# Kernel tuning notes

Measured on AMD Instinct MI355X. Metric: run time of the kernel, lower is better.

## Reference

```python
import jax, jax.numpy as jnp
import numpy as np
from jax import lax

B, CIN, COUT, K, MOD, BANK = 4, 64, 32, 3, 128, 4
D = H = W = 32
EPS = 1e-8


def _lin_upsample2x(x, axis):
    n = x.shape[axis]
    dst = jnp.arange(2 * n, dtype=jnp.float32)
    src = jnp.maximum((dst + 0.5) * 0.5 - 0.5, 0.0)
    i0 = jnp.floor(src).astype(jnp.int32)
    i1 = jnp.minimum(i0 + 1, n - 1)
    w1 = src - i0.astype(jnp.float32)
    shape = [1] * x.ndim
    shape[axis] = 2 * n
    w1 = w1.reshape(shape)
    return jnp.take(x, i0, axis=axis) * (1.0 - w1) + jnp.take(x, i1, axis=axis) * w1


def upsample_trilinear2x(x):
    for ax in (2, 3, 4):
        x = _lin_upsample2x(x, ax)
    return x


def setup_inputs() -> dict:
    key = jax.random.key(0)
    ks = jax.random.split(key, 9)
    fan = CIN * K * K * K
    return {
        "x": jax.random.normal(ks[0], (B, CIN, D, H, W), jnp.float32),
        "style": jax.random.normal(ks[1], (B, MOD), jnp.float32),
        "bank": jax.random.normal(ks[2], (BANK, COUT, CIN, K, K, K), jnp.float32) / np.sqrt(fan),
        "affine_w": jax.random.normal(ks[3], (CIN, MOD), jnp.float32) / np.sqrt(MOD),
        "affine_b": jnp.ones((CIN,), jnp.float32),  # StyleGAN bias init = 1
        "sel_w": jax.random.normal(ks[4], (BANK, MOD), jnp.float32) / np.sqrt(MOD),
        "sel_b": jnp.zeros((BANK,), jnp.float32),
        "vox_w": jax.random.normal(ks[5], (1, COUT), jnp.float32) / np.sqrt(COUT),
        "vox_b": jnp.zeros((1,), jnp.float32),
    }


def reference(x, style, bank, affine_w, affine_b, sel_w, sel_b, vox_w, vox_b):
    # --- AdaptiveModulatedConv3d: select kernel from bank, modulate, demodulate ---
    alpha = jax.nn.softmax(style @ sel_w.T + sel_b, axis=-1)            # [B, BANK]
    w = jnp.einsum('bn,noidhw->boidhw', alpha, bank)                    # per-sample kernel
    s = style @ affine_w.T + affine_b                                   # [B, CIN]
    w = w * s[:, None, :, None, None, None]                             # modulate
    demod = lax.rsqrt(jnp.sum(w * w, axis=(2, 3, 4, 5)) + EPS)          # [B, COUT]
    w = w * demod[:, :, None, None, None, None]

    def conv1(xi, wi):
        return lax.conv_general_dilated(
            xi[None], wi, window_strides=(1, 1, 1),
            padding=[(1, 1), (1, 1), (1, 1)],
            dimension_numbers=('NCDHW', 'OIDHW', 'NCDHW'))[0]

    y = jax.vmap(conv1)(x, w)                                           # [B, COUT, D, H, W]

    y = upsample_trilinear2x(y)                                         # [B, COUT, 2D, 2H, 2W]

    # --- VoxelizingBlock: 1x1x1 conv to 1 channel ---
    out = jnp.einsum('oc,bcdhw->bodhw', vox_w, y) + vox_b[None, :, None, None, None]
    return (y, out)
```

## Files before the change

kernel.cpp:

```cpp
#include <hip/hip_runtime.h>
#include <math.h>

#define B_    4
#define CIN_  64
#define COUT_ 32
#define MOD_  128
#define VOX_  32768
#define UPVOX_ 262144
#define TAPS_ 27
#define EPS_  1e-8f

#define HALO_   1224
#define XUNITS_ 2448
#define CHUNK_HALVES_ 13824

#define WS_WF16  512
#define WS_Y     111104
#define WS_V32   4305408

#define OUT_YUP  0
#define OUT_VOX  33554432

typedef _Float16 half8 __attribute__((ext_vector_type(8)));
typedef float floatx16 __attribute__((ext_vector_type(16)));
typedef float floatx4 __attribute__((ext_vector_type(4)));

__global__ __launch_bounds__(256) void k_prep(
    const float* __restrict__ x,
    const float* __restrict__ style,
    const float* __restrict__ bank,
    const float* __restrict__ affine_w,
    const float* __restrict__ affine_b,
    const float* __restrict__ sel_w,
    const float* __restrict__ sel_b,
    _Float16* __restrict__ xt,
    _Float16* __restrict__ wf) {
  __shared__ float red[256];
  __shared__ float sS[64];
  __shared__ float sLg[4];
  __shared__ float sAl[4];
  const int tid = threadIdx.x;

  if (blockIdx.z == 4) {
    const int sid = blockIdx.y * 34 + blockIdx.x;
    if (sid >= 128) return;
    const int b = sid >> 5;
    const int o = sid & 31;
    const float* st = style + b * MOD_;

    if (tid < 64) {
      float v = affine_b[tid];
      for (int k = 0; k < MOD_; ++k) v += st[k] * affine_w[tid * MOD_ + k];
      sS[tid] = v;
    } else if (tid < 68) {
      const int n = tid - 64;
      float l = sel_b[n];
      for (int k = 0; k < MOD_; ++k) l += st[k] * sel_w[n * MOD_ + k];
      sLg[n] = l;
    }
    __syncthreads();
    if (tid < 4) {
      const float m = fmaxf(fmaxf(sLg[0], sLg[1]), fmaxf(sLg[2], sLg[3]));
      float den = 0.f;
      for (int j = 0; j < 4; ++j) den += expf(sLg[j] - m);
      sAl[tid] = expf(sLg[tid] - m) / den;
    }
    __syncthreads();

    float al[4];
#pragma unroll
    for (int n = 0; n < 4; ++n) al[n] = sAl[n];

    float wv[7];
    float ss = 0.f;
#pragma unroll
    for (int r = 0; r < 7; ++r) {
      const int e = tid + r * 256;
      float v = 0.f;
      if (e < CIN_ * TAPS_) {
        const int i = e / TAPS_;
        const int t = e - i * TAPS_;
        const int base = (o * CIN_ + i) * TAPS_ + t;
        float bw = 0.f;
#pragma unroll
        for (int n = 0; n < 4; ++n)
          bw += al[n] * bank[base + n * (COUT_ * CIN_ * TAPS_)];
        v = bw * sS[i];
      }
      wv[r] = v;
      ss += v * v;
    }
    red[tid] = ss;
    __syncthreads();
    for (int stg = 128; stg > 0; stg >>= 1) {
      if (tid < stg) red[tid] += red[tid + stg];
      __syncthreads();
    }
    const float demod = rsqrtf(red[0] + EPS_);

#pragma unroll
    for (int r = 0; r < 7; ++r) {
      const int e = tid + r * 256;
      if (e < CIN_ * TAPS_) {
        const int i = e / TAPS_;
        const int t = e - i * TAPS_;
        const int c = i >> 4, h = (i >> 3) & 1, j = i & 7;
        wf[((((b * 4 + c) * TAPS_ + t) * 2 + h) * 32 + o) * 8 + j] =
            (_Float16)(wv[r] * demod);
      }
    }
    return;
  }

  const int yp = blockIdx.x, zp = blockIdx.y, b = blockIdx.z;
  const int gz = zp - 1, gy = yp - 1;
  const bool zy_ok = ((unsigned)gz < 32u) && ((unsigned)gy < 32u);
  const int gzc = min(max(gz, 0), 31);
  const int gyc = min(max(gy, 0), 31);
  _Float16* dst = xt + (((size_t)(b * 34 + zp) * 34 + yp) * 34) * 64;
  const float* srow = x + ((size_t)b * CIN_) * VOX_ + gzc * 1024 + gyc * 32;
  for (int u = tid; u < 34 * 8; u += 256) {
    const int xp = u >> 3, q = u & 7;
    const int gx = xp - 1;
    const bool ok = zy_ok && ((unsigned)gx < 32u);
    const float m = ok ? 1.0f : 0.0f;
    const int gxc = min(max(gx, 0), 31);
    half8 h;
#pragma unroll
    for (int i = 0; i < 8; ++i) {
      const float v = srow[(size_t)(q * 8 + i) * VOX_ + gxc];
      h[i] = (_Float16)(v * m);
    }
    *(half8*)&dst[xp * 64 + q * 8] = h;
  }
}

__global__ __launch_bounds__(256, 1) void k_conv(
    const _Float16* __restrict__ xt,
    const _Float16* __restrict__ wf,
    const float* __restrict__ vox_w,
    float* __restrict__ ws_y,
    float* __restrict__ v32) {
  __shared__ __align__(16) _Float16 xs[2][XUNITS_ * 8];

  const int b  = blockIdx.y;
  const int bx = blockIdx.x;
  const int z0 = (bx >> 3) * 4;
  const int y0 = (bx & 7) * 4;
  const int tid = threadIdx.x;
  const int w = tid >> 6;
  const int lane = tid & 63;
  const int hf = lane >> 5;
  const int col = lane & 31;
  const int wz = (w >> 1) * 2;
  const int wy = (w & 1) * 2;

  const _Float16* xtb = xt + (size_t)b * (34 * 34 * 34 * 64);
  const _Float16* wfb = wf + (size_t)b * 4 * CHUNK_HALVES_;
  const _Float16* wlane = wfb + ((size_t)(hf * 32 + col)) * 8;

  int xoff[10];
  bool xok[10];
#pragma unroll
  for (int j = 0; j < 10; ++j) {
    const int u = j * 256 + tid;
    xok[j] = (u < XUNITS_);
    const int uc = xok[j] ? u : 0;
    const int h = uc / HALO_, hv = uc - h * HALO_;
    const int hz = hv / 204;
    const int rem = hv - hz * 204;
    const int hy = rem / 34;
    const int hx = rem - hy * 34;
    xoff[j] = (((z0 + hz) * 34 + (y0 + hy)) * 34 + hx) * 64 + h * 8;
  }

  floatx16 acc[2][2];
#pragma unroll
  for (int az = 0; az < 2; ++az)
#pragma unroll
    for (int ay = 0; ay < 2; ++ay)
#pragma unroll
      for (int r = 0; r < 16; ++r) acc[az][ay][r] = 0.f;

  half8 xv[10], afv[27];

  auto load_af = [&](int c) {
#pragma unroll
    for (int t = 0; t < TAPS_; ++t)
      afv[t] = *(const half8*)(wlane + (size_t)c * CHUNK_HALVES_ + t * 512);
  };
  auto load_chunk = [&](int c) {
#pragma unroll
    for (int j = 0; j < 10; ++j)
      xv[j] = *(const half8*)(xtb + xoff[j] + c * 16);
  };
  auto write_chunk = [&](int bufi) {
#pragma unroll
    for (int j = 0; j < 10; ++j) {
      const int u = j * 256 + tid;
      if (xok[j]) *(half8*)&xs[bufi][u * 8] = xv[j];
    }
  };
  auto compute = [&](int bufi) {
    const _Float16* xb_ = xs[bufi];
#pragma unroll
    for (int dx = 0; dx < 3; ++dx) {
      half8 Bf[4][4];
#pragma unroll
      for (int zs = 0; zs < 4; ++zs)
#pragma unroll
        for (int ys = 0; ys < 4; ++ys) {
          const int hv = ((wz + zs) * 6 + (wy + ys)) * 34 + dx + col;
          Bf[zs][ys] = *(const half8*)&xb_[(hf * HALO_ + hv) * 8];
        }
#pragma unroll
      for (int dz = 0; dz < 3; ++dz)
#pragma unroll
        for (int dy = 0; dy < 3; ++dy) {
          const half8 af = afv[(dz * 3 + dy) * 3 + dx];
          acc[0][0] = __builtin_amdgcn_mfma_f32_32x32x16_f16(af, Bf[dz][dy], acc[0][0], 0, 0, 0);
          acc[0][1] = __builtin_amdgcn_mfma_f32_32x32x16_f16(af, Bf[dz][dy + 1], acc[0][1], 0, 0, 0);
          acc[1][0] = __builtin_amdgcn_mfma_f32_32x32x16_f16(af, Bf[dz + 1][dy], acc[1][0], 0, 0, 0);
          acc[1][1] = __builtin_amdgcn_mfma_f32_32x32x16_f16(af, Bf[dz + 1][dy + 1], acc[1][1], 0, 0, 0);
        }
    }
  };

  load_af(0);
  load_chunk(0);
  write_chunk(0);
  __syncthreads();
  for (int c = 0; c < 4; ++c) {
    if (c < 3) load_chunk(c + 1);
    compute(c & 1);
    if (c < 3) {
      load_af(c + 1);
      write_chunk((c + 1) & 1);
      __syncthreads();
    }
  }

  float vw[16];
#pragma unroll
  for (int r = 0; r < 16; ++r)
    vw[r] = vox_w[(r & 3) + 8 * (r >> 2) + 4 * hf];

  float* yb2 = ws_y + (size_t)b * COUT_ * VOX_;
#pragma unroll
  for (int az = 0; az < 2; ++az)
#pragma unroll
    for (int ay = 0; ay < 2; ++ay) {
      const int zz = z0 + wz + az, yy = y0 + wy + ay;
      const int vbase = zz * 1024 + yy * 32 + col;
      float p = 0.f;
#pragma unroll
      for (int r = 0; r < 16; ++r) {
        const int oc = (r & 3) + 8 * (r >> 2) + 4 * hf;
        yb2[(size_t)oc * VOX_ + vbase] = acc[az][ay][r];
        p = fmaf(vw[r], acc[az][ay][r], p);
      }
      p += __shfl_xor(p, 32);
      if (hf == 0) v32[((size_t)b << 15) + vbase] = p;
    }
}

__global__ __launch_bounds__(256) void k_up(
    const float* __restrict__ ws_y,
    const float* __restrict__ v32,
    const float* __restrict__ vox_b,
    float* __restrict__ out) {
  __shared__ float P[4][1056];
  const int kq = blockIdx.x;
  const int ch = blockIdx.y;
  const int b = blockIdx.z;

  const float* src = (ch < 32) ? (ws_y + (((size_t)(b * 32 + ch)) << 15))
                               : (v32 + ((size_t)b << 15));
  for (int j = threadIdx.x; j < 1024; j += 256) {
    const int p = j >> 8, idx = j & 255;
    const int r = idx >> 3, q = (idx & 7) * 4;
    const int zsrc = min(max(2 * kq - 1 + p, 0), 31);
    const float4 v = *(const float4*)(src + (zsrc << 10) + r * 32 + q);
    float* dp = &P[p][r * 33 + q];
    dp[0] = v.x; dp[1] = v.y; dp[2] = v.z; dp[3] = v.w;
  }
  __syncthreads();

  const int yp = threadIdx.x >> 3;
  const int xq = threadIdx.x & 7;
  const int ym = max(yp - 1, 0) * 33, yc = yp * 33, ypp = min(yp + 1, 31) * 33;

  int gxi[6];
#pragma unroll
  for (int i = 0; i < 6; ++i) gxi[i] = min(max(4 * xq - 1 + i, 0), 31);

  const float vb = (ch == 32) ? vox_b[0] : 0.f;
  float* base0 = out + ((ch < 32) ? (OUT_YUP + (((size_t)(b * 32 + ch)) * UPVOX_))
                                  : (OUT_VOX + (size_t)b * UPVOX_)) +
                 (2 * yp) * 64 + 8 * xq;

#pragma unroll
  for (int zi = 0; zi < 2; ++zi) {
    float ry[3][2][6];
#pragma unroll
    for (int p = 0; p < 3; ++p)
#pragma unroll
      for (int i = 0; i < 6; ++i) {
        const float a = P[zi + p][ym + gxi[i]];
        const float bb = P[zi + p][yc + gxi[i]];
        const float cc = P[zi + p][ypp + gxi[i]];
        ry[p][0][i] = fmaf(0.25f, a, 0.75f * bb);
        ry[p][1][i] = fmaf(0.25f, cc, 0.75f * bb);
      }

    float* base = base0 + (size_t)(2 * (2 * kq + zi)) * 4096;
#pragma unroll
    for (int zo = 0; zo < 2; ++zo)
#pragma unroll
      for (int yo = 0; yo < 2; ++yo) {
        float s[6];
#pragma unroll
        for (int i = 0; i < 6; ++i)
          s[i] = zo == 0 ? fmaf(0.25f, ry[0][yo][i], 0.75f * ry[1][yo][i])
                         : fmaf(0.25f, ry[2][yo][i], 0.75f * ry[1][yo][i]);
        float o[8];
#pragma unroll
        for (int ox = 0; ox < 8; ++ox) {
          const int k = ox >> 1;
          o[ox] = (ox & 1) ? fmaf(0.25f, s[k + 2], 0.75f * s[k + 1])
                           : fmaf(0.25f, s[k], 0.75f * s[k + 1]);
          o[ox] += vb;
        }
        float* dst = base + (size_t)zo * 4096 + yo * 64;
        floatx4 v0; v0.x = o[0]; v0.y = o[1]; v0.z = o[2]; v0.w = o[3];
        floatx4 v1; v1.x = o[4]; v1.y = o[5]; v1.z = o[6]; v1.w = o[7];
        __builtin_nontemporal_store(v0, (floatx4*)dst);
        __builtin_nontemporal_store(v1, (floatx4*)(dst + 4));
      }
  }
}

extern "C" void kernel_launch(void* const* d_in, const int* in_sizes, int n_in,
                              void* d_out, int out_size, void* d_ws, size_t ws_size,
                              hipStream_t stream) {
  const float* x        = (const float*)d_in[0];
  const float* style    = (const float*)d_in[1];
  const float* bank     = (const float*)d_in[2];
  const float* affine_w = (const float*)d_in[3];
  const float* affine_b = (const float*)d_in[4];
  const float* sel_w    = (const float*)d_in[5];
  const float* sel_b    = (const float*)d_in[6];
  const float* vox_w    = (const float*)d_in[7];
  const float* vox_b    = (const float*)d_in[8];
  float* out = (float*)d_out;
  float* ws  = (float*)d_ws;
  _Float16* wf16 = (_Float16*)(ws + WS_WF16);
  float* ws_y = ws + WS_Y;
  float* v32  = ws + WS_V32;
  _Float16* xt = (_Float16*)d_out;

  k_prep<<<dim3(34, 34, 5), 256, 0, stream>>>(x, style, bank, affine_w, affine_b,
                                              sel_w, sel_b, xt, wf16);
  k_conv<<<dim3(64, B_), 256, 0, stream>>>(xt, wf16, vox_w, ws_y, v32);
  k_up<<<dim3(16, 33, B_), 256, 0, stream>>>(ws_y, v32, vox_b, out);
}
```

Measured before the change: 258.7 us.

## Halve conv z-tile to double block count and occupancy; use plain stores in upsample

The conv kernel now gives each block 2 z-slices instead of 4, so each wave holds two accumulators instead of four and the grid grows from 256 to 512 blocks. Launch bounds allow two blocks per CU, and the shared-memory halo shrinks to match. This aims to spread the work across all CUs and raise occupancy, at the cost of a larger relative halo (more redundant input and weight loads per output). Separately, the upsample kernel switches from nontemporal stores to ordinary float4 stores.

```diff
diff --git a/kernel.cpp b/kernel.cpp
--- a/kernel.cpp
+++ b/kernel.cpp
@@ -10,8 +10,8 @@
 #define TAPS_ 27
 #define EPS_  1e-8f
 
-#define HALO_   1224
-#define XUNITS_ 2448
+#define HALO_   816
+#define XUNITS_ 1632
 #define CHUNK_HALVES_ 13824
 
 #define WS_WF16  512
@@ -23,7 +23,6 @@
 
 typedef _Float16 half8 __attribute__((ext_vector_type(8)));
 typedef float floatx16 __attribute__((ext_vector_type(16)));
-typedef float floatx4 __attribute__((ext_vector_type(4)));
 
 __global__ __launch_bounds__(256) void k_prep(
     const float* __restrict__ x,
@@ -135,7 +134,7 @@
   }
 }
 
-__global__ __launch_bounds__(256, 1) void k_conv(
+__global__ __launch_bounds__(256, 2) void k_conv(
     const _Float16* __restrict__ xt,
     const _Float16* __restrict__ wf,
     const float* __restrict__ vox_w,
@@ -145,24 +144,24 @@
 
   const int b  = blockIdx.y;
   const int bx = blockIdx.x;
-  const int z0 = (bx >> 3) * 4;
+  const int z0 = (bx >> 3) * 2;
   const int y0 = (bx & 7) * 4;
   const int tid = threadIdx.x;
   const int w = tid >> 6;
   const int lane = tid & 63;
   const int hf = lane >> 5;
   const int col = lane & 31;
-  const int wz = (w >> 1) * 2;
+  const int wz = w >> 1;
   const int wy = (w & 1) * 2;
 
   const _Float16* xtb = xt + (size_t)b * (34 * 34 * 34 * 64);
   const _Float16* wfb = wf + (size_t)b * 4 * CHUNK_HALVES_;
   const _Float16* wlane = wfb + ((size_t)(hf * 32 + col)) * 8;
 
-  int xoff[10];
-  bool xok[10];
-#pragma unroll
-  for (int j = 0; j < 10; ++j) {
+  int xoff[7];
+  bool xok[7];
+#pragma unroll
+  for (int j = 0; j < 7; ++j) {
     const int u = j * 256 + tid;
     xok[j] = (u < XUNITS_);
     const int uc = xok[j] ? u : 0;
@@ -174,15 +173,13 @@
     xoff[j] = (((z0 + hz) * 34 + (y0 + hy)) * 34 + hx) * 64 + h * 8;
   }
 
-  floatx16 acc[2][2];
-#pragma unroll
-  for (int az = 0; az < 2; ++az)
-#pragma unroll
-    for (int ay = 0; ay < 2; ++ay)
-#pragma unroll
-      for (int r = 0; r < 16; ++r) acc[az][ay][r] = 0.f;
-
-  half8 xv[10], afv[27];
+  floatx16 acc[2];
+#pragma unroll
+  for (int ay = 0; ay < 2; ++ay)
+#pragma unroll
+    for (int r = 0; r < 16; ++r) acc[ay][r] = 0.f;
+
+  half8 xv[7], afv[27];
 
   auto load_af = [&](int c) {
 #pragma unroll
@@ -191,12 +188,12 @@
   };
   auto load_chunk = [&](int c) {
 #pragma unroll
-    for (int j = 0; j < 10; ++j)
+    for (int j = 0; j < 7; ++j)
       xv[j] = *(const half8*)(xtb + xoff[j] + c * 16);
   };
   auto write_chunk = [&](int bufi) {
 #pragma unroll
-    for (int j = 0; j < 10; ++j) {
+    for (int j = 0; j < 7; ++j) {
       const int u = j * 256 + tid;
       if (xok[j]) *(half8*)&xs[bufi][u * 8] = xv[j];
     }
@@ -205,9 +202,9 @@
     const _Float16* xb_ = xs[bufi];
 #pragma unroll
     for (int dx = 0; dx < 3; ++dx) {
-      half8 Bf[4][4];
-#pragma unroll
-      for (int zs = 0; zs < 4; ++zs)
+      half8 Bf[3][4];
+#pragma unroll
+      for (int zs = 0; zs < 3; ++zs)
 #pragma unroll
         for (int ys = 0; ys < 4; ++ys) {
           const int hv = ((wz + zs) * 6 + (wy + ys)) * 34 + dx + col;
@@ -218,10 +215,8 @@
 #pragma unroll
         for (int dy = 0; dy < 3; ++dy) {
           const half8 af = afv[(dz * 3 + dy) * 3 + dx];
-          acc[0][0] = __builtin_amdgcn_mfma_f32_32x32x16_f16(af, Bf[dz][dy], acc[0][0], 0, 0, 0);
-          acc[0][1] = __builtin_amdgcn_mfma_f32_32x32x16_f16(af, Bf[dz][dy + 1], acc[0][1], 0, 0, 0);
-          acc[1][0] = __builtin_amdgcn_mfma_f32_32x32x16_f16(af, Bf[dz + 1][dy], acc[1][0], 0, 0, 0);
-          acc[1][1] = __builtin_amdgcn_mfma_f32_32x32x16_f16(af, Bf[dz + 1][dy + 1], acc[1][1], 0, 0, 0);
+          acc[0] = __builtin_amdgcn_mfma_f32_32x32x16_f16(af, Bf[dz][dy], acc[0], 0, 0, 0);
+          acc[1] = __builtin_amdgcn_mfma_f32_32x32x16_f16(af, Bf[dz][dy + 1], acc[1], 0, 0, 0);
         }
     }
   };
@@ -247,21 +242,19 @@
 
   float* yb2 = ws_y + (size_t)b * COUT_ * VOX_;
 #pragma unroll
-  for (int az = 0; az < 2; ++az)
-#pragma unroll
-    for (int ay = 0; ay < 2; ++ay) {
-      const int zz = z0 + wz + az, yy = y0 + wy + ay;
-      const int vbase = zz * 1024 + yy * 32 + col;
-      float p = 0.f;
-#pragma unroll
-      for (int r = 0; r < 16; ++r) {
-        const int oc = (r & 3) + 8 * (r >> 2) + 4 * hf;
-        yb2[(size_t)oc * VOX_ + vbase] = acc[az][ay][r];
-        p = fmaf(vw[r], acc[az][ay][r], p);
-      }
-      p += __shfl_xor(p, 32);
-      if (hf == 0) v32[((size_t)b << 15) + vbase] = p;
-    }
+  for (int ay = 0; ay < 2; ++ay) {
+    const int zz = z0 + wz, yy = y0 + wy + ay;
+    const int vbase = zz * 1024 + yy * 32 + col;
+    float p = 0.f;
+#pragma unroll
+    for (int r = 0; r < 16; ++r) {
+      const int oc = (r & 3) + 8 * (r >> 2) + 4 * hf;
+      yb2[(size_t)oc * VOX_ + vbase] = acc[ay][r];
+      p = fmaf(vw[r], acc[ay][r], p);
+    }
+    p += __shfl_xor(p, 32);
+    if (hf == 0) v32[((size_t)b << 15) + vbase] = p;
+  }
 }
 
 __global__ __launch_bounds__(256) void k_up(
@@ -331,11 +324,11 @@
                            : fmaf(0.25f, s[k], 0.75f * s[k + 1]);
           o[ox] += vb;
         }
-        float* dst = base + (size_t)zo * 4096 + yo * 64;
-        floatx4 v0; v0.x = o[0]; v0.y = o[1]; v0.z = o[2]; v0.w = o[3];
-        floatx4 v1; v1.x = o[4]; v1.y = o[5]; v1.z = o[6]; v1.w = o[7];
-        __builtin_nontemporal_store(v0, (floatx4*)dst);
-        __builtin_nontemporal_store(v1, (floatx4*)(dst + 4));
+        float4* dst = (float4*)(base + (size_t)zo * 4096 + yo * 64);
+        float4 v0; v0.x = o[0]; v0.y = o[1]; v0.z = o[2]; v0.w = o[3];
+        float4 v1; v1.x = o[4]; v1.y = o[5]; v1.z = o[6]; v1.w = o[7];
+        dst[0] = v0;
+        dst[1] = v1;
       }
   }
 }
@@ -361,6 +354,6 @@
 
   k_prep<<<dim3(34, 34, 5), 256, 0, stream>>>(x, style, bank, affine_w, affine_b,
                                               sel_w, sel_b, xt, wf16);
-  k_conv<<<dim3(64, B_), 256, 0, stream>>>(xt, wf16, vox_w, ws_y, v32);
+  k_conv<<<dim3(128, B_), 256, 0, stream>>>(xt, wf16, vox_w, ws_y, v32);
   k_up<<<dim3(16, 33, B_), 256, 0, stream>>>(ws_y, v32, vox_b, out);
 }
```

After: 222.8 us. 13.9% less time.
